# Optimization experiments

Measured on AMD Instinct MI355X. Metric: run time of the kernel, lower is better.

The kernel has to match this reference:

```python
import jax, jax.numpy as jnp
import numpy as np


def setup_inputs() -> dict:
    key = jax.random.key(0)
    k0, k1, k2, k3 = jax.random.split(key, 4)
    B, S, D, F, E = 8, 2048, 1024, 2048, 8
    x = jax.random.normal(k0, (B, S, D), dtype=jnp.float32)
    Wg = jax.random.normal(k1, (D, E), dtype=jnp.float32) * 0.02
    W1 = jax.random.normal(k2, (E, D, F), dtype=jnp.float32) * 0.02
    W2 = jax.random.normal(k3, (E, F, D), dtype=jnp.float32) * 0.02
    return {"x": x, "Wg": Wg, "W1": W1, "W2": W2}


def reference(x, Wg, W1, W2):
    # Expert-choice MoE: experts pick top-C tokens, conflicts resolved by
    # max router prob (ties -> lowest expert index, matching the serial loop).
    B, S, D = x.shape
    E = Wg.shape[1]
    T = B * S
    cap = max(1, T // E)  # capacity_factor = 1.0

    xt = x.reshape(T, D)
    logits = xt @ Wg                      # [T, E]
    probs = jax.nn.softmax(logits, axis=-1)
    pT = probs.T                          # [E, T] token affinities per expert

    _, top_idx = jax.lax.top_k(pT, cap)   # [E, cap] tokens chosen by each expert
    sel = jnp.zeros((E, T), dtype=bool).at[jnp.arange(E)[:, None], top_idx].set(True)

    # Serial conflict loop is equivalent to: per token, pick the selecting
    masked = jnp.where(sel, pT, -jnp.inf)
    assigned = sel.any(axis=0)            # [T]
    tok2exp = jnp.where(assigned,
                        jnp.argmax(masked, axis=0),
                        jnp.argmax(pT, axis=0))          # [T] int
    weights = jnp.take_along_axis(probs, tok2exp[:, None], axis=1)[:, 0]  # [T]

    # Dispatch / expert FFN / weighted combine. Loop over the small fixed
    # expert set; masked tokens contribute exactly zero, matching index_add_.
    out = jnp.zeros_like(xt)
    for e in range(E):
        gate = jnp.where(tok2exp == e, weights, 0.0)     # [T]
        h = jax.nn.gelu(xt @ W1[e], approximate=False) @ W2[e]  # [T, D]
        out = out + gate[:, None] * h

    return out.reshape(B, S, D)
```

## Files before the change

### kernel.cpp

```cpp
#include <hip/hip_runtime.h>
#include <hip/hip_bf16.h>
#include <math.h>

#define T_TOK 16384
#define DIM   1024
#define FF    2048
#define NE    8
#define CAPK  2048
#define MTE_MAX 16
#define WL1SZ (NE * 8 * MTE_MAX)
#define WL2SZ (NE * 4 * MTE_MAX)

typedef unsigned short u16;
typedef unsigned long long u64;
typedef __attribute__((ext_vector_type(8))) short bf16x8;
typedef __attribute__((ext_vector_type(4))) float f32x4;

__device__ __forceinline__ u16 f2bf(float f) {
  __hip_bfloat16 h = __float2bfloat16(f);
  union { __hip_bfloat16 h; u16 u; } c; c.h = h; return c.u;
}

__device__ __forceinline__ float gelu_f(float v) {
  float z = fabsf(v) * 0.70710678118654752f;
  float t = __builtin_amdgcn_rcpf(1.0f + 0.3275911f * z);
  float poly = t * (0.254829592f +
               t * (-0.284496736f +
               t * (1.421413741f +
               t * (-1.453152027f +
               t * 1.061405429f))));
  float ez = __expf(-z * z);
  float erfz = 1.0f - poly * ez;
  erfz = copysignf(erfz, v);
  return 0.5f * v * (1.0f + erfz);
}

__device__ __forceinline__ void async_copy16(const void* g, void* l) {
  __builtin_amdgcn_global_load_lds(
      (const __attribute__((address_space(1))) unsigned int*)g,
      (__attribute__((address_space(3))) unsigned int*)l, 16, 0, 0);
}

__device__ __forceinline__ bf16x8 ds_read16(const char* p) {
  bf16x8 r;
  asm volatile("ds_read_b128 %0, %1"
               : "=&v"(r)
               : "v"((const __attribute__((address_space(3))) char*)p));
  return r;
}

__global__ __launch_bounds__(256) void transpose_cvt(const float* __restrict__ src,
                                                     u16* __restrict__ dst, int R, int C) {
  __shared__ float tile[32][35];
  int e = blockIdx.z;
  int c0 = blockIdx.x * 32, r0 = blockIdx.y * 32;
  const float* s = src + (size_t)e * R * C;
  u16* d = dst + (size_t)e * R * C;
  int tid = threadIdx.x;
#pragma unroll
  for (int i = 0; i < 4; ++i) {
    int idx = tid + i * 256;
    int r = idx >> 5, c = idx & 31;
    tile[r][c] = s[(size_t)(r0 + r) * C + c0 + c];
  }
  __syncthreads();
  int q = tid & 7, cc = tid >> 3;
  ushort4 h;
  h.x = f2bf(tile[q * 4 + 0][cc]);
  h.y = f2bf(tile[q * 4 + 1][cc]);
  h.z = f2bf(tile[q * 4 + 2][cc]);
  h.w = f2bf(tile[q * 4 + 3][cc]);
  *(ushort4*)(d + (size_t)(c0 + cc) * R + r0 + q * 4) = h;
}

__global__ __launch_bounds__(256) void router_k(const float* __restrict__ x,
                                                const float* __restrict__ Wg,
                                                float* __restrict__ probs,
                                                float* __restrict__ probsT,
                                                u16* __restrict__ xb,
                                                u64* __restrict__ key,
                                                int* cnt, int* cnt2) {
  int tid = threadIdx.x;
  if (tid < 4) key[blockIdx.x * 4 + tid] = 0ull;
  if (blockIdx.x == 0 && tid < NE) { cnt[tid] = 0; cnt2[tid] = 0; }
  int wid = tid >> 6, lane = tid & 63;
  int t = blockIdx.x * 4 + wid;
  const float* xr = x + (size_t)t * DIM;
  u16* xbr = xb + (size_t)t * DIM;
  double acc[NE] = {0, 0, 0, 0, 0, 0, 0, 0};
#pragma unroll 1
  for (int it = 0; it < DIM / 64; ++it) {
    int d = it * 64 + lane;
    float xv = xr[d];
    xbr[d] = f2bf(xv);
    const float4* wrow = (const float4*)(Wg + (size_t)d * NE);
    float4 w0 = wrow[0], w1 = wrow[1];
    acc[0] += (double)xv * (double)w0.x;
    acc[1] += (double)xv * (double)w0.y;
    acc[2] += (double)xv * (double)w0.z;
    acc[3] += (double)xv * (double)w0.w;
    acc[4] += (double)xv * (double)w1.x;
    acc[5] += (double)xv * (double)w1.y;
    acc[6] += (double)xv * (double)w1.z;
    acc[7] += (double)xv * (double)w1.w;
  }
#pragma unroll
  for (int e = 0; e < NE; ++e)
    for (int o = 32; o > 0; o >>= 1) acc[e] += __shfl_down(acc[e], o, 64);
  if (lane == 0) {
    float l[NE], mx = -3.0e38f;
#pragma unroll
    for (int e = 0; e < NE; ++e) { l[e] = (float)acc[e]; mx = fmaxf(mx, l[e]); }
    float s = 0.f;
#pragma unroll
    for (int e = 0; e < NE; ++e) { l[e] = expf(l[e] - mx); s += l[e]; }
    float inv = 1.0f / s;
#pragma unroll
    for (int e = 0; e < NE; ++e) {
      float p = l[e] * inv;
      probs[(size_t)t * NE + e] = p;
      probsT[(size_t)e * T_TOK + t] = p;
    }
  }
}

__global__ __launch_bounds__(256) void topk_sel(const float* __restrict__ probsT,
                                                u64* __restrict__ key) {
  __shared__ float pcol[T_TOK];
  __shared__ unsigned whist[8][2048];
  __shared__ unsigned hist[2048];
  __shared__ unsigned bcast[2];
  __shared__ unsigned wsum[4];
  __shared__ int wps[4];
  int e = blockIdx.x, tid = threadIdx.x, wid = tid >> 6, lane = tid & 63;
  const float4* src4 = (const float4*)(probsT + (size_t)e * T_TOK);
  for (int i = tid; i < T_TOK / 4; i += 256) ((float4*)pcol)[i] = src4[i];
  for (int i = tid; i < 8 * 2048; i += 256) ((unsigned*)whist)[i] = 0;
  unsigned prefix = 0, remaining = CAPK;
#pragma unroll 1
  for (int lvl = 0; lvl < 3; ++lvl) {
    int nb = (lvl == 2) ? 1024 : 2048;
    if (lvl == 0) {
      __syncthreads();
      for (int i = tid; i < T_TOK; i += 256)
        atomicAdd(&whist[wid][__float_as_uint(pcol[i]) >> 21], 1u);
      __syncthreads();
      for (int j = tid; j < 2048; j += 256) {
        unsigned s2 = 0;
#pragma unroll
        for (int w = 0; w < 8; ++w) s2 += whist[w][j];
        hist[j] = s2;
      }
      __syncthreads();
    } else {
      for (int i = tid; i < 2048; i += 256) hist[i] = 0;
      __syncthreads();
      for (int i = tid; i < T_TOK; i += 256) {
        unsigned k = __float_as_uint(pcol[i]);
        bool m = (lvl == 1) ? ((k >> 21) == prefix) : ((k >> 10) == prefix);
        if (m) atomicAdd(&hist[(lvl == 1) ? ((k >> 10) & 2047u) : (k & 1023u)], 1u);
      }
      __syncthreads();
    }
    int nper = nb / 256;
    unsigned cv = 0;
    for (int j = 0; j < nper; ++j) cv += hist[tid * nper + j];
    unsigned s = cv;
#pragma unroll
    for (int o = 1; o < 64; o <<= 1) {
      unsigned tv = __shfl_down(s, o, 64);
      if (lane + o < 64) s += tv;
    }
    if (lane == 0) wsum[wid] = s;
    __syncthreads();
    unsigned above = 0;
    for (int w = wid + 1; w < 4; ++w) above += wsum[w];
    unsigned Sincl = s + above, Sexcl = Sincl - cv;
    if (Sincl >= remaining && Sexcl < remaining) {
      unsigned rem2 = remaining - Sexcl, cum2 = 0;
      for (int j = nper - 1; j >= 0; --j) {
        unsigned h = hist[tid * nper + j];
        if (cum2 + h >= rem2) { bcast[0] = (unsigned)(tid * nper + j); bcast[1] = rem2 - cum2; break; }
        cum2 += h;
      }
    }
    __syncthreads();
    unsigned b = bcast[0];
    remaining = bcast[1];
    prefix = (lvl == 0) ? b : (lvl == 1) ? ((prefix << 11) | b) : ((prefix << 10) | b);
    __syncthreads();
  }
  unsigned vk = prefix;
  int need = (int)remaining;
  const int CH = T_TOK / 256;
  int i0 = tid * CH;
  int myt = 0;
  for (int i = i0; i < i0 + CH; ++i)
    myt += (__float_as_uint(pcol[i]) == vk);
  int p = myt;
#pragma unroll
  for (int o = 1; o < 64; o <<= 1) {
    int tv = __shfl_up(p, o, 64);
    if (lane >= o) p += tv;
  }
  if (lane == 63) wps[wid] = p;
  __syncthreads();
  int wo = 0;
  for (int w = 0; w < wid; ++w) wo += wps[w];
  int run = wo + p - myt;
  u64 ebits = (u64)(7 - e);
  for (int i = i0; i < i0 + CH; ++i) {
    unsigned k = __float_as_uint(pcol[i]);
    bool sv = false;
    if (k > vk) sv = true;
    else if (k == vk) { if (run < need) sv = true; run++; }
    if (sv) atomicMax(&key[i], ((u64)k << 3) | ebits);
  }
}

__global__ __launch_bounds__(256) void assign_k(const float* __restrict__ probs,
                                                const u64* __restrict__ key,
                                                int* __restrict__ tok2exp,
                                                float* __restrict__ wgt, int* cnt) {
  int t = blockIdx.x * 256 + threadIdx.x;
  int lane = threadIdx.x & 63;
  u64 k = key[t];
  int best;
  float bp;
  if (k) {
    best = 7 - (int)(k & 7);
    bp = __uint_as_float((unsigned)(k >> 3));
  } else {
    best = 0; bp = -3.0e38f;
#pragma unroll
    for (int e = 0; e < NE; ++e) {
      float p = probs[(size_t)t * NE + e];
      if (p > bp) { bp = p; best = e; }
    }
  }
  tok2exp[t] = best;
  wgt[t] = bp;
#pragma unroll
  for (int e = 0; e < NE; ++e) {
    u64 m = __ballot(best == e);
    if (best == e && lane == __ffsll(m) - 1) atomicAdd(&cnt[e], (int)__popcll(m));
  }
}

__global__ __launch_bounds__(256) void slot_wl_k(const int* __restrict__ tok2exp,
                                                 const int* __restrict__ cnt,
                                                 int* cnt2, int* __restrict__ list,
                                                 int* basep, int* wl1, int* wl2) {
  int gid = blockIdx.x * 256 + threadIdx.x;
  int lane = threadIdx.x & 63;
  int c[NE];
#pragma unroll
  for (int e = 0; e < NE; ++e) c[e] = cnt[e];
  if (gid < NE) {
    int r = 0;
    for (int e = 0; e < gid; ++e) r += c[e];
    basep[gid] = r;
  }
  if (gid < WL1SZ) {
    int e = gid & 7, j = gid >> 3;
    int mte = (c[e] + 255) >> 8;
    int v = -1;
    if (j < 8 * mte) {
      int half = 4 * mte;
      int h = (j >= half) ? 1 : 0;
      int jj = j - h * half;
      v = e | ((jj >> 2) << 4) | (((h << 2) | (jj & 3)) << 12);
    }
    wl1[gid] = v;
  }
  if (gid >= WL1SZ && gid < WL1SZ + WL2SZ) {
    int g2 = gid - WL1SZ;
    int e = g2 & 7, j = g2 >> 3;
    int mte = (c[e] + 255) >> 8;
    int v = -1;
    if (j < 4 * mte) {
      int half = 2 * mte;
      int h = (j >= half) ? 1 : 0;
      int jj = j - h * half;
      v = e | ((jj >> 1) << 4) | (((h << 1) | (jj & 1)) << 12);
    }
    wl2[g2] = v;
  }
  int te = tok2exp[gid];
  int bp_e = 0;
#pragma unroll
  for (int e = 0; e < NE; ++e) if (e < te) bp_e += c[e];
  int sl = 0;
#pragma unroll
  for (int e = 0; e < NE; ++e) {
    u64 m = __ballot(te == e);
    if (te == e) {
      int leader = __ffsll(m) - 1;
      int rank = __popcll(m & ((1ull << lane) - 1));
      int b = 0;
      if (lane == leader) b = atomicAdd(&cnt2[e], (int)__popcll(m));
      b = __shfl(b, leader, 64);
      sl = bp_e + b + rank;
    }
  }
  list[sl] = gid;
}


#define MF(M, N_, AV, BV) acc[M][N_] = __builtin_amdgcn_mfma_f32_16x16x32_bf16(BV, AV, acc[M][N_], 0, 0, 0)

#define SLOT_A(s) (sm + (s) * 32768)
#define SLOT_B(s) (sm + (s) * 32768 + 16384)

#define PHASE_DSA(s, mh)                                                          \
  pa = SLOT_A(s) + wr * 8192 + (mh) * 4096 + laneOff;                             \
  a0 = ds_read16(pa);                                                             \
  a1 = ds_read16(pa + 1024);                                                      \
  a2 = ds_read16(pa + 2048);                                                      \
  a3 = ds_read16(pa + 3072);

#define PHASE_DSB(s)                                                              \
  pb = SLOT_B(s) + wc * 4096 + laneOff;                                           \
  b0 = ds_read16(pb);                                                             \
  b1 = ds_read16(pb + 1024);                                                      \
  b2 = ds_read16(pb + 2048);                                                      \
  b3 = ds_read16(pb + 3072);

#define WAIT_LGKM()                                                               \
  do {                                                                            \
    asm volatile("s_waitcnt lgkmcnt(0)" ::: "memory");                            \
    __builtin_amdgcn_sched_barrier(0);                                            \
  } while (0)

#define PHASE_MFMA(mh)                                                            \
  do {                                                                            \
    __builtin_amdgcn_s_setprio(1);                                                \
    MF((mh) * 4 + 0, 0, a0, b0); MF((mh) * 4 + 0, 1, a0, b1);                     \
    MF((mh) * 4 + 0, 2, a0, b2); MF((mh) * 4 + 0, 3, a0, b3);                     \
    MF((mh) * 4 + 1, 0, a1, b0); MF((mh) * 4 + 1, 1, a1, b1);                     \
    MF((mh) * 4 + 1, 2, a1, b2); MF((mh) * 4 + 1, 3, a1, b3);                     \
    MF((mh) * 4 + 2, 0, a2, b0); MF((mh) * 4 + 2, 1, a2, b1);                     \
    MF((mh) * 4 + 2, 2, a2, b2); MF((mh) * 4 + 2, 3, a2, b3);                     \
    MF((mh) * 4 + 3, 0, a3, b0); MF((mh) * 4 + 3, 1, a3, b1);                     \
    MF((mh) * 4 + 3, 2, a3, b2); MF((mh) * 4 + 3, 3, a3, b3);                     \
    __builtin_amdgcn_s_setprio(0);                                                \
  } while (0)

#define STAGE_A(s, kt)                                                            \
  do {                                                                            \
    async_copy16(aP0 + (size_t)(kt) * 64, SLOT_A(s) + wid * 1024);                \
    async_copy16(aP1 + (size_t)(kt) * 64, SLOT_A(s) + 8192 + wid * 1024);         \
  } while (0)

#define STAGE_B(s, kt)                                                            \
  do {                                                                            \
    async_copy16(bP0 + (size_t)(kt) * 64, SLOT_B(s) + wid * 1024);                \
    async_copy16(bP1 + (size_t)(kt) * 64, SLOT_B(s) + 8192 + wid * 1024);         \
  } while (0)

#define BAR() asm volatile("s_barrier" ::: "memory")

template <int EPI>
__global__ __launch_bounds__(512, 2) void ffn_k(const u16* __restrict__ A,
                                                const u16* __restrict__ Bm,
                                                void* __restrict__ Out,
                                                const int* __restrict__ list,
                                                const float* __restrict__ wgt,
                                                const int* __restrict__ basep,
                                                const int* __restrict__ cnt,
                                                const int* __restrict__ wl) {
  constexpr int K = EPI ? FF : DIM;
  constexpr int N = EPI ? DIM : FF;
  constexpr int KT = K / 32;

  const int wle = wl[blockIdx.x];
  if (wle < 0) return;
  const int e = wle & 15, mt = (wle >> 4) & 255, nt = wle >> 12;
  const int ce = cnt[e];
  const int be = basep[e];

  __shared__ u16 smem[65536];
  __shared__ int toks[256];
  __shared__ float wsc[256];
  char* const sm = (char*)smem;

  const int tid = threadIdx.x;
  if (tid < 256) {
    int r = mt * 256 + tid;
    int tk = (r < ce) ? list[be + r] : list[be];
    toks[tid] = tk;
    if (EPI == 1) wsc[tid] = wgt[tk];
  }
  __syncthreads();

  const int wid = tid >> 6, lane = tid & 63;
  const int wr = wid >> 2, wc = wid & 3;
  const int laneOff = ((lane & 15) >> 1) * 128 + (lane & 1) * 64 +
                      (((lane >> 4) << 4) ^ (((lane >> 1) & 3) << 4));

  const int tr0 = ((tid >> 3) << 1) + ((tid >> 2) & 1), tr1 = 128 + tr0;
  const int cbl = ((tid & 3) << 4) ^ (((tid >> 3) & 3) << 4);
  const char *aP0, *aP1;
  if (EPI == 0) {
    aP0 = (const char*)(A + (size_t)toks[tr0] * K) + cbl;
    aP1 = (const char*)(A + (size_t)toks[tr1] * K) + cbl;
  } else {
    aP0 = (const char*)(A + ((size_t)be + mt * 256 + tr0) * K) + cbl;
    aP1 = (const char*)(A + ((size_t)be + mt * 256 + tr1) * K) + cbl;
  }
  const char* bP0 = (const char*)(Bm + ((size_t)e * N + nt * 256 + tr0) * K) + cbl;
  const char* bP1 = (const char*)(Bm + ((size_t)e * N + nt * 256 + tr1) * K) + cbl;

  f32x4 acc[8][4];
#pragma unroll
  for (int m = 0; m < 8; ++m)
#pragma unroll
    for (int n = 0; n < 4; ++n) acc[m][n] = (f32x4){0.f, 0.f, 0.f, 0.f};

  STAGE_A(0, 0); STAGE_B(0, 0);
  STAGE_A(1, 1); STAGE_B(1, 1);
  STAGE_A(2, 2); STAGE_B(2, 2);
  asm volatile("s_waitcnt vmcnt(8)" ::: "memory");
  BAR();

  const char* pa;
  const char* pb;
  bf16x8 a0, a1, a2, a3, b0, b1, b2, b3;

#pragma unroll 1
  for (int kt = 0; kt < KT; ++kt) {
    const int s = kt & 3, sn = (kt + 3) & 3;
    const bool pf = (kt + 3 < KT);
    if (pf) STAGE_A(sn, kt + 3);
    PHASE_DSA(s, 0);
    PHASE_DSB(s);
    BAR();
    WAIT_LGKM();
    PHASE_MFMA(0);
    if (pf) STAGE_B(sn, kt + 3);
    PHASE_DSA(s, 1);
    if (kt < KT - 3)       asm volatile("s_waitcnt vmcnt(8)" ::: "memory");
    else if (kt == KT - 3) asm volatile("s_waitcnt vmcnt(4)" ::: "memory");
    else if (kt == KT - 2) asm volatile("s_waitcnt vmcnt(0)" ::: "memory");
    BAR();
    WAIT_LGKM();
    PHASE_MFMA(1);
  }

  const int lc = lane & 15, lq = (lane >> 4) * 4;
#pragma unroll
  for (int m = 0; m < 8; ++m) {
    int trow = wr * 128 + m * 16 + lc;
    int grow = mt * 256 + trow;
    if (grow < ce) {
      if (EPI == 0) {
        size_t rowoff = (size_t)(be + grow) * FF + nt * 256 + wc * 64 + lq;
#pragma unroll
        for (int n = 0; n < 4; ++n) {
          ushort4 h4;
          h4.x = f2bf(gelu_f(acc[m][n][0]));
          h4.y = f2bf(gelu_f(acc[m][n][1]));
          h4.z = f2bf(gelu_f(acc[m][n][2]));
          h4.w = f2bf(gelu_f(acc[m][n][3]));
          *(ushort4*)((u16*)Out + rowoff + n * 16) = h4;
        }
      } else {
        float w = wsc[trow];
        size_t rowoff = (size_t)toks[trow] * DIM + nt * 256 + wc * 64 + lq;
#pragma unroll
        for (int n = 0; n < 4; ++n) {
          float4 o = make_float4(w * acc[m][n][0], w * acc[m][n][1],
                                 w * acc[m][n][2], w * acc[m][n][3]);
          *(float4*)((float*)Out + rowoff + n * 16) = o;
        }
      }
    }
  }
}

extern "C" void kernel_launch(void* const* d_in, const int* in_sizes, int n_in,
                              void* d_out, int out_size, void* d_ws, size_t ws_size,
                              hipStream_t stream) {
  (void)in_sizes; (void)n_in; (void)out_size; (void)ws_size;
  const float* x  = (const float*)d_in[0];
  const float* Wg = (const float*)d_in[1];
  const float* W1 = (const float*)d_in[2];
  const float* W2 = (const float*)d_in[3];
  float* out = (float*)d_out;

  char* ws = (char*)d_ws;
  size_t off = 0;
  auto alloc = [&](size_t bytes) -> void* {
    void* p = ws + off;
    off += (bytes + 255) & ~(size_t)255;
    return p;
  };
  u16* xb   = (u16*)alloc((size_t)T_TOK * DIM * 2);
  u16* w1t  = (u16*)alloc((size_t)NE * FF * DIM * 2);
  u16* w2t  = (u16*)alloc((size_t)NE * DIM * FF * 2);
  u16* H    = (u16*)alloc((size_t)(T_TOK + 256) * FF * 2);
  float* probs  = (float*)alloc((size_t)T_TOK * NE * 4);
  float* probsT = (float*)alloc((size_t)NE * T_TOK * 4);
  u64* key      = (u64*)alloc((size_t)T_TOK * 8);
  float* wgt    = (float*)alloc((size_t)T_TOK * 4);
  int* tok2exp  = (int*)alloc((size_t)T_TOK * 4);
  int* list     = (int*)alloc((size_t)T_TOK * 4);
  int* cnt      = (int*)alloc(64);
  int* cnt2     = (int*)alloc(64);
  int* basep    = (int*)alloc(64);
  int* wl1      = (int*)alloc(WL1SZ * 4);
  int* wl2      = (int*)alloc(WL2SZ * 4);

  transpose_cvt<<<dim3(FF / 32, DIM / 32, NE), 256, 0, stream>>>(W1, w1t, DIM, FF);
  transpose_cvt<<<dim3(DIM / 32, FF / 32, NE), 256, 0, stream>>>(W2, w2t, FF, DIM);
  router_k<<<T_TOK / 4, 256, 0, stream>>>(x, Wg, probs, probsT, xb, key, cnt, cnt2);
  topk_sel<<<NE, 256, 0, stream>>>(probsT, key);
  assign_k<<<T_TOK / 256, 256, 0, stream>>>(probs, key, tok2exp, wgt, cnt);
  slot_wl_k<<<T_TOK / 256, 256, 0, stream>>>(tok2exp, cnt, cnt2, list, basep, wl1, wl2);
  ffn_k<0><<<WL1SZ, 512, 0, stream>>>(xb, w1t, H, list, wgt, basep, cnt, wl1);
  ffn_k<1><<<WL2SZ, 512, 0, stream>>>(H, w2t, out, list, wgt, basep, cnt, wl2);
}
```

Measured before the change: 397.2 us.

## Software-pipeline LDS reads across k-tiles in FFN GEMM and merge weight transposes

The FFN GEMM main loop is restructured so the next k-tile's B fragments and low A fragments are read from LDS while the current tile's upper MFMAs run. It uses double-buffered B registers and partial lgkmcnt waits, with one barrier per k-tile instead of two. The aim is to hide LDS latency and cut barrier stalls, at the cost of more VGPRs, which could hurt occupancy at 2 waves per SIMD. Separately, the two weight transpose-convert kernels are merged into one launch that uses 64x64 tiles, float4 loads and 16-byte stores.

```diff
diff --git a/kernel.cpp b/kernel.cpp
--- a/kernel.cpp
+++ b/kernel.cpp
@@ -49,28 +49,40 @@
   return r;
 }
 
-__global__ __launch_bounds__(256) void transpose_cvt(const float* __restrict__ src,
-                                                     u16* __restrict__ dst, int R, int C) {
-  __shared__ float tile[32][35];
-  int e = blockIdx.z;
-  int c0 = blockIdx.x * 32, r0 = blockIdx.y * 32;
-  const float* s = src + (size_t)e * R * C;
-  u16* d = dst + (size_t)e * R * C;
+__global__ __launch_bounds__(256) void transpose_cvt2(const float* __restrict__ W1,
+                                                      const float* __restrict__ W2,
+                                                      u16* __restrict__ w1t,
+                                                      u16* __restrict__ w2t) {
+  __shared__ float tile[64][65];
+  int z = blockIdx.y;
+  const float* src;
+  u16* dst;
+  int R, C;
+  if (z < 8) { src = W1 + (size_t)z * DIM * FF; dst = w1t + (size_t)z * DIM * FF; R = DIM; C = FF; }
+  else       { src = W2 + (size_t)(z - 8) * FF * DIM; dst = w2t + (size_t)(z - 8) * FF * DIM; R = FF; C = DIM; }
+  int nbx = C >> 6;
+  int bx = blockIdx.x % nbx, by = blockIdx.x / nbx;
+  int r0 = by * 64, c0 = bx * 64;
   int tid = threadIdx.x;
-#pragma unroll
-  for (int i = 0; i < 4; ++i) {
-    int idx = tid + i * 256;
-    int r = idx >> 5, c = idx & 31;
-    tile[r][c] = s[(size_t)(r0 + r) * C + c0 + c];
+  int lr = tid >> 4, lc4 = (tid & 15) * 4;
+#pragma unroll
+  for (int p = 0; p < 4; ++p) {
+    float4 v = *(const float4*)(src + (size_t)(r0 + p * 16 + lr) * C + c0 + lc4);
+    tile[p * 16 + lr][lc4 + 0] = v.x;
+    tile[p * 16 + lr][lc4 + 1] = v.y;
+    tile[p * 16 + lr][lc4 + 2] = v.z;
+    tile[p * 16 + lr][lc4 + 3] = v.w;
   }
   __syncthreads();
-  int q = tid & 7, cc = tid >> 3;
-  ushort4 h;
-  h.x = f2bf(tile[q * 4 + 0][cc]);
-  h.y = f2bf(tile[q * 4 + 1][cc]);
-  h.z = f2bf(tile[q * 4 + 2][cc]);
-  h.w = f2bf(tile[q * 4 + 3][cc]);
-  *(ushort4*)(d + (size_t)(c0 + cc) * R + r0 + q * 4) = h;
+  int oc = tid >> 3, orr = (tid & 7) * 8;
+#pragma unroll
+  for (int p = 0; p < 2; ++p) {
+    int c = p * 32 + oc;
+    u16 h[8];
+#pragma unroll
+    for (int j = 0; j < 8; ++j) h[j] = f2bf(tile[orr + j][c]);
+    *(uint4*)(dst + (size_t)(c0 + c) * R + r0 + orr) = *(uint4*)h;
+  }
 }
 
 __global__ __launch_bounds__(256) void router_k(const float* __restrict__ x,
@@ -312,37 +324,47 @@
 #define SLOT_A(s) (sm + (s) * 32768)
 #define SLOT_B(s) (sm + (s) * 32768 + 16384)
 
-#define PHASE_DSA(s, mh)                                                          \
-  pa = SLOT_A(s) + wr * 8192 + (mh) * 4096 + laneOff;                             \
-  a0 = ds_read16(pa);                                                             \
-  a1 = ds_read16(pa + 1024);                                                      \
-  a2 = ds_read16(pa + 2048);                                                      \
-  a3 = ds_read16(pa + 3072);
-
-#define PHASE_DSB(s)                                                              \
+#define DSA_LO(s)                                                                 \
+  pa = SLOT_A(s) + wr * 8192 + laneOff;                                           \
+  a0 = ds_read16(pa);        a1 = ds_read16(pa + 1024);                           \
+  a2 = ds_read16(pa + 2048); a3 = ds_read16(pa + 3072);
+
+#define DSA_HI(s)                                                                 \
+  pa = SLOT_A(s) + wr * 8192 + 4096 + laneOff;                                    \
+  a4 = ds_read16(pa);        a5 = ds_read16(pa + 1024);                           \
+  a6 = ds_read16(pa + 2048); a7 = ds_read16(pa + 3072);
+
+#define DSB_RD(s, BP)                                                             \
   pb = SLOT_B(s) + wc * 4096 + laneOff;                                           \
-  b0 = ds_read16(pb);                                                             \
-  b1 = ds_read16(pb + 1024);                                                      \
-  b2 = ds_read16(pb + 2048);                                                      \
-  b3 = ds_read16(pb + 3072);
-
-#define WAIT_LGKM()                                                               \
+  BP##0 = ds_read16(pb);        BP##1 = ds_read16(pb + 1024);                     \
+  BP##2 = ds_read16(pb + 2048); BP##3 = ds_read16(pb + 3072);
+
+#define LGKM(n)                                                                   \
   do {                                                                            \
-    asm volatile("s_waitcnt lgkmcnt(0)" ::: "memory");                            \
+    asm volatile("s_waitcnt lgkmcnt(" #n ")" ::: "memory");                       \
     __builtin_amdgcn_sched_barrier(0);                                            \
   } while (0)
 
-#define PHASE_MFMA(mh)                                                            \
+#define VMW(n) asm volatile("s_waitcnt vmcnt(" #n ")" ::: "memory")
+#define BAR() asm volatile("s_barrier" ::: "memory")
+
+#define MFMA_LO(BP)                                                               \
   do {                                                                            \
     __builtin_amdgcn_s_setprio(1);                                                \
-    MF((mh) * 4 + 0, 0, a0, b0); MF((mh) * 4 + 0, 1, a0, b1);                     \
-    MF((mh) * 4 + 0, 2, a0, b2); MF((mh) * 4 + 0, 3, a0, b3);                     \
-    MF((mh) * 4 + 1, 0, a1, b0); MF((mh) * 4 + 1, 1, a1, b1);                     \
-    MF((mh) * 4 + 1, 2, a1, b2); MF((mh) * 4 + 1, 3, a1, b3);                     \
-    MF((mh) * 4 + 2, 0, a2, b0); MF((mh) * 4 + 2, 1, a2, b1);                     \
-    MF((mh) * 4 + 2, 2, a2, b2); MF((mh) * 4 + 2, 3, a2, b3);                     \
-    MF((mh) * 4 + 3, 0, a3, b0); MF((mh) * 4 + 3, 1, a3, b1);                     \
-    MF((mh) * 4 + 3, 2, a3, b2); MF((mh) * 4 + 3, 3, a3, b3);                     \
+    MF(0, 0, a0, BP##0); MF(0, 1, a0, BP##1); MF(0, 2, a0, BP##2); MF(0, 3, a0, BP##3); \
+    MF(1, 0, a1, BP##0); MF(1, 1, a1, BP##1); MF(1, 2, a1, BP##2); MF(1, 3, a1, BP##3); \
+    MF(2, 0, a2, BP##0); MF(2, 1, a2, BP##1); MF(2, 2, a2, BP##2); MF(2, 3, a2, BP##3); \
+    MF(3, 0, a3, BP##0); MF(3, 1, a3, BP##1); MF(3, 2, a3, BP##2); MF(3, 3, a3, BP##3); \
+    __builtin_amdgcn_s_setprio(0);                                                \
+  } while (0)
+
+#define MFMA_HI(BP)                                                               \
+  do {                                                                            \
+    __builtin_amdgcn_s_setprio(1);                                                \
+    MF(4, 0, a4, BP##0); MF(4, 1, a4, BP##1); MF(4, 2, a4, BP##2); MF(4, 3, a4, BP##3); \
+    MF(5, 0, a5, BP##0); MF(5, 1, a5, BP##1); MF(5, 2, a5, BP##2); MF(5, 3, a5, BP##3); \
+    MF(6, 0, a6, BP##0); MF(6, 1, a6, BP##1); MF(6, 2, a6, BP##2); MF(6, 3, a6, BP##3); \
+    MF(7, 0, a7, BP##0); MF(7, 1, a7, BP##1); MF(7, 2, a7, BP##2); MF(7, 3, a7, BP##3); \
     __builtin_amdgcn_s_setprio(0);                                                \
   } while (0)
 
@@ -358,7 +380,27 @@
     async_copy16(bP1 + (size_t)(kt) * 64, SLOT_B(s) + 8192 + wid * 1024);         \
   } while (0)
 
-#define BAR() asm volatile("s_barrier" ::: "memory")
+#define TILE_KT(kt, BCUR, BNXT)                                                   \
+  do {                                                                            \
+    const int sC = (kt) & 3, sP = ((kt) + 3) & 3, sN = ((kt) + 1) & 3;            \
+    if ((kt) + 3 < KT) STAGE_A(sP, (kt) + 3);                                     \
+    DSA_HI(sC);                                                                   \
+    LGKM(4);                                                                      \
+    MFMA_LO(BCUR);                                                                \
+    if ((kt) + 3 < KT) STAGE_B(sP, (kt) + 3);                                     \
+    if ((kt) < KT - 1) {                                                          \
+      if ((kt) < KT - 3)        { VMW(8); }                                       \
+      else if ((kt) == KT - 3)  { VMW(4); }                                       \
+      else                      { VMW(0); }                                       \
+      BAR();                                                                      \
+      DSB_RD(sN, BNXT);                                                           \
+      DSA_LO(sN);                                                                 \
+      LGKM(8);                                                                    \
+    } else {                                                                      \
+      LGKM(0);                                                                    \
+    }                                                                             \
+    MFMA_HI(BCUR);                                                                \
+  } while (0)
 
 template <int EPI>
 __global__ __launch_bounds__(512, 2) void ffn_k(const u16* __restrict__ A,
@@ -420,31 +462,21 @@
   STAGE_A(0, 0); STAGE_B(0, 0);
   STAGE_A(1, 1); STAGE_B(1, 1);
   STAGE_A(2, 2); STAGE_B(2, 2);
-  asm volatile("s_waitcnt vmcnt(8)" ::: "memory");
+  VMW(8);
   BAR();
 
   const char* pa;
   const char* pb;
-  bf16x8 a0, a1, a2, a3, b0, b1, b2, b3;
+  bf16x8 a0, a1, a2, a3, a4, a5, a6, a7;
+  bf16x8 bA0, bA1, bA2, bA3, bB0, bB1, bB2, bB3;
+
+  DSB_RD(0, bA);
+  DSA_LO(0);
 
 #pragma unroll 1
-  for (int kt = 0; kt < KT; ++kt) {
-    const int s = kt & 3, sn = (kt + 3) & 3;
-    const bool pf = (kt + 3 < KT);
-    if (pf) STAGE_A(sn, kt + 3);
-    PHASE_DSA(s, 0);
-    PHASE_DSB(s);
-    BAR();
-    WAIT_LGKM();
-    PHASE_MFMA(0);
-    if (pf) STAGE_B(sn, kt + 3);
-    PHASE_DSA(s, 1);
-    if (kt < KT - 3)       asm volatile("s_waitcnt vmcnt(8)" ::: "memory");
-    else if (kt == KT - 3) asm volatile("s_waitcnt vmcnt(4)" ::: "memory");
-    else if (kt == KT - 2) asm volatile("s_waitcnt vmcnt(0)" ::: "memory");
-    BAR();
-    WAIT_LGKM();
-    PHASE_MFMA(1);
+  for (int kt = 0; kt < KT; kt += 2) {
+    TILE_KT(kt, bA, bB);
+    TILE_KT(kt + 1, bB, bA);
   }
 
   const int lc = lane & 15, lq = (lane >> 4) * 4;
@@ -511,8 +543,7 @@
   int* wl1      = (int*)alloc(WL1SZ * 4);
   int* wl2      = (int*)alloc(WL2SZ * 4);
 
-  transpose_cvt<<<dim3(FF / 32, DIM / 32, NE), 256, 0, stream>>>(W1, w1t, DIM, FF);
-  transpose_cvt<<<dim3(DIM / 32, FF / 32, NE), 256, 0, stream>>>(W2, w2t, FF, DIM);
+  transpose_cvt2<<<dim3(512, 16), 256, 0, stream>>>(W1, W2, w1t, w2t);
   router_k<<<T_TOK / 4, 256, 0, stream>>>(x, Wg, probs, probsT, xb, key, cnt, cnt2);
   topk_sel<<<NE, 256, 0, stream>>>(probsT, key);
   assign_k<<<T_TOK / 256, 256, 0, stream>>>(probs, key, tok2exp, wgt, cnt);
```

New measurement: 386.7 us. -2.7%, faster.
